# Kernel tuning notes

Hardware: AMD Instinct MI355X
Metric: run time of the kernel (lower is better)

The kernel has to match this reference:

```python
import jax, jax.numpy as jnp
import numpy as np

N_GENES = 20000
UNITS = 10000
DEG = 32
BATCH = 128

def setup_inputs() -> dict:
    key = jax.random.key(0)
    k1, k2, k3, k4 = jax.random.split(key, 4)
    feature = jax.random.normal(k1, (BATCH, N_GENES), dtype=jnp.float32)
    ppi = jax.random.randint(k2, (UNITS, DEG), 0, N_GENES, dtype=jnp.int64)
    kernel = jax.random.normal(k3, (UNITS,), dtype=jnp.float32)
    bias = jax.random.normal(k4, (UNITS,), dtype=jnp.float32)
    return {"feature": feature, "ppi": ppi, "kernel": kernel, "bias": bias}

def reference(feature, ppi, kernel, bias):
    # gather along gene axis: [B, UNITS, DEG]
    h = jnp.abs(feature[:, ppi])
    # sum over neighbors -> [B, UNITS]
    h = jnp.sum(h, axis=-1)
    h = h * kernel + bias
    return jnp.tanh(h)
```

## Files before the change

### kernel.cpp

```cpp
#include <hip/hip_runtime.h>
#include <hip/hip_fp16.h>
#include <math.h>

#define N_GENES 20000
#define UNITS   10000
#define DEG     32
#define BATCH   128

__global__ __launch_bounds__(256) void transpose_abs_f16_kernel(
    const float* __restrict__ in, __half* __restrict__ out)
{
    __shared__ float tile[32][33];
    const int g0 = blockIdx.x * 32;
    const int b0 = blockIdx.y * 32;
    const int tx = threadIdx.x;
    const int ty = threadIdx.y;
#pragma unroll
    for (int i = 0; i < 32; i += 8)
        tile[ty + i][tx] = fabsf(in[(size_t)(b0 + ty + i) * N_GENES + (g0 + tx)]);
    __syncthreads();
#pragma unroll
    for (int i = 0; i < 32; i += 8)
        out[(size_t)(g0 + ty + i) * BATCH + (b0 + tx)] = __float2half(tile[tx][ty + i]);
}

__global__ __launch_bounds__(256) void gather_unit_kernel(
    const __half2* __restrict__ featT,
    const int*   __restrict__ ppi,
    const float* __restrict__ kernelw,
    const float* __restrict__ bias,
    float*       __restrict__ out)
{
    __shared__ int idx[8 * DEG];
    const int tid = threadIdx.x;
    const int u0  = blockIdx.x * 8;

    idx[tid] = ppi[(size_t)u0 * DEG + tid];
    __syncthreads();

    const int lane = tid & 63;
    const int w    = tid >> 6;
    const int ub   = w * 2;

    float2 acc0 = {0.f, 0.f}, acc1 = {0.f, 0.f};

#pragma unroll 8
    for (int d = 0; d < DEG; ++d) {
        const int g0 = idx[ub * DEG + d];
        const int g1 = idx[(ub + 1) * DEG + d];
        const float2 f0 = __half22float2(featT[(size_t)g0 * 64 + lane]);
        const float2 f1 = __half22float2(featT[(size_t)g1 * 64 + lane]);
        acc0.x += f0.x; acc0.y += f0.y;
        acc1.x += f1.x; acc1.y += f1.y;
    }

    const int u  = u0 + ub;
    const float k0 = kernelw[u],     k1 = kernelw[u + 1];
    const float c0 = bias[u],        c1 = bias[u + 1];

    const float h00 = acc0.x * k0 + c0;
    const float h01 = acc1.x * k1 + c1;
    const float h10 = acc0.y * k0 + c0;
    const float h11 = acc1.y * k1 + c1;
    const float r00 = 1.f - 2.f / (__expf(2.f * h00) + 1.f);
    const float r01 = 1.f - 2.f / (__expf(2.f * h01) + 1.f);
    const float r10 = 1.f - 2.f / (__expf(2.f * h10) + 1.f);
    const float r11 = 1.f - 2.f / (__expf(2.f * h11) + 1.f);

    const int b = lane * 2;
    *(float2*)(out + (size_t)b       * UNITS + u) = make_float2(r00, r01);
    *(float2*)(out + (size_t)(b + 1) * UNITS + u) = make_float2(r10, r11);
}

extern "C" void kernel_launch(void* const* d_in, const int* in_sizes, int n_in,
                              void* d_out, int out_size, void* d_ws, size_t ws_size,
                              hipStream_t stream) {
    const float* feature = (const float*)d_in[0];
    const int*   ppi     = (const int*)d_in[1];
    const float* kernelw = (const float*)d_in[2];
    const float* bias    = (const float*)d_in[3];
    float* out   = (float*)d_out;
    __half* featT = (__half*)d_ws;

    dim3 g1(N_GENES / 32, BATCH / 32);
    dim3 b1(32, 8);
    transpose_abs_f16_kernel<<<g1, b1, 0, stream>>>(feature, featT);

    gather_unit_kernel<<<UNITS / 8, 256, 0, stream>>>(
        (const __half2*)featT, ppi, kernelw, bias, out);
}
```

Measured before the change: 78.83 us.

## Split transposed features into batch halves and gather with 8-byte loads per lane

```diff
diff --git a/kernel.cpp b/kernel.cpp
--- a/kernel.cpp
+++ b/kernel.cpp
@@ -6,6 +6,7 @@
 #define UNITS   10000
 #define DEG     32
 #define BATCH   128
+
 
 __global__ __launch_bounds__(256) void transpose_abs_f16_kernel(
     const float* __restrict__ in, __half* __restrict__ out)
@@ -19,12 +20,17 @@
     for (int i = 0; i < 32; i += 8)
         tile[ty + i][tx] = fabsf(in[(size_t)(b0 + ty + i) * N_GENES + (g0 + tx)]);
     __syncthreads();
+    const int b  = b0 + tx;
+    const int p  = b >> 6;
+    const int bh = b & 63;
 #pragma unroll
-    for (int i = 0; i < 32; i += 8)
-        out[(size_t)(g0 + ty + i) * BATCH + (b0 + tx)] = __float2half(tile[tx][ty + i]);
+    for (int i = 0; i < 32; i += 8) {
+        const int g = g0 + ty + i;
+        out[((size_t)p * N_GENES + g) * 64 + bh] = __float2half(tile[tx][ty + i]);
+    }
 }
 
-__global__ __launch_bounds__(256) void gather_unit_kernel(
+__global__ __launch_bounds__(256) void gather_unit_v3(
     const __half2* __restrict__ featT,
     const int*   __restrict__ ppi,
     const float* __restrict__ kernelw,
@@ -40,36 +46,44 @@
 
     const int lane = tid & 63;
     const int w    = tid >> 6;
-    const int ub   = w * 2;
+    const int dpar = lane >> 5;
+    const int ul   = w * 2 + ((lane >> 4) & 1);
+    const int bq   = lane & 15;
+    const int u    = u0 + ul;
+    const float kk = kernelw[u];
+    const float cc = bias[u];
+    const int* myidx = idx + ul * DEG;
 
-    float2 acc0 = {0.f, 0.f}, acc1 = {0.f, 0.f};
+#pragma unroll
+    for (int p = 0; p < 2; ++p) {
+        const uint2* fp = reinterpret_cast<const uint2*>(featT) + (size_t)p * N_GENES * 16;
+        float acc0 = 0.f, acc1 = 0.f, acc2 = 0.f, acc3 = 0.f;
+#pragma unroll
+        for (int t = 0; t < 16; ++t) {
+            const int d = 2 * t + dpar;
+            const int g = myidx[d];
+            const uint2 raw = fp[(size_t)g * 16 + bq];
+            const float2 f0 = __half22float2(*reinterpret_cast<const __half2*>(&raw.x));
+            const float2 f1 = __half22float2(*reinterpret_cast<const __half2*>(&raw.y));
+            acc0 += f0.x; acc1 += f0.y; acc2 += f1.x; acc3 += f1.y;
+        }
+        acc0 += __shfl_xor(acc0, 32, 64);
+        acc1 += __shfl_xor(acc1, 32, 64);
+        acc2 += __shfl_xor(acc2, 32, 64);
+        acc3 += __shfl_xor(acc3, 32, 64);
 
-#pragma unroll 8
-    for (int d = 0; d < DEG; ++d) {
-        const int g0 = idx[ub * DEG + d];
-        const int g1 = idx[(ub + 1) * DEG + d];
-        const float2 f0 = __half22float2(featT[(size_t)g0 * 64 + lane]);
-        const float2 f1 = __half22float2(featT[(size_t)g1 * 64 + lane]);
-        acc0.x += f0.x; acc0.y += f0.y;
-        acc1.x += f1.x; acc1.y += f1.y;
+        if (dpar == 0) {
+            const int bbase = p * 64 + bq * 4;
+            const float h0 = acc0 * kk + cc;
+            const float h1 = acc1 * kk + cc;
+            const float h2 = acc2 * kk + cc;
+            const float h3 = acc3 * kk + cc;
+            out[(size_t)(bbase + 0) * UNITS + u] = 1.f - 2.f / (__expf(2.f * h0) + 1.f);
+            out[(size_t)(bbase + 1) * UNITS + u] = 1.f - 2.f / (__expf(2.f * h1) + 1.f);
+            out[(size_t)(bbase + 2) * UNITS + u] = 1.f - 2.f / (__expf(2.f * h2) + 1.f);
+            out[(size_t)(bbase + 3) * UNITS + u] = 1.f - 2.f / (__expf(2.f * h3) + 1.f);
+        }
     }
-
-    const int u  = u0 + ub;
-    const float k0 = kernelw[u],     k1 = kernelw[u + 1];
-    const float c0 = bias[u],        c1 = bias[u + 1];
-
-    const float h00 = acc0.x * k0 + c0;
-    const float h01 = acc1.x * k1 + c1;
-    const float h10 = acc0.y * k0 + c0;
-    const float h11 = acc1.y * k1 + c1;
-    const float r00 = 1.f - 2.f / (__expf(2.f * h00) + 1.f);
-    const float r01 = 1.f - 2.f / (__expf(2.f * h01) + 1.f);
-    const float r10 = 1.f - 2.f / (__expf(2.f * h10) + 1.f);
-    const float r11 = 1.f - 2.f / (__expf(2.f * h11) + 1.f);
-
-    const int b = lane * 2;
-    *(float2*)(out + (size_t)b       * UNITS + u) = make_float2(r00, r01);
-    *(float2*)(out + (size_t)(b + 1) * UNITS + u) = make_float2(r10, r11);
 }
 
 extern "C" void kernel_launch(void* const* d_in, const int* in_sizes, int n_in,
@@ -86,6 +100,6 @@
     dim3 b1(32, 8);
     transpose_abs_f16_kernel<<<g1, b1, 0, stream>>>(feature, featT);
 
-    gather_unit_kernel<<<UNITS / 8, 256, 0, stream>>>(
+    gather_unit_v3<<<UNITS / 8, 256, 0, stream>>>(
         (const __half2*)featT, ppi, kernelw, bias, out);
 }
```

Result: no change. 78.57 us (-0.3%).

## Fuse abs/fp16 conversion into gather by staging batch-row pairs in LDS

Applied to the files above, without the earlier changes.

```diff
diff --git a/kernel.cpp b/kernel.cpp
--- a/kernel.cpp
+++ b/kernel.cpp
@@ -7,69 +7,59 @@
 #define DEG     32
 #define BATCH   128
 
-__global__ __launch_bounds__(256) void transpose_abs_f16_kernel(
-    const float* __restrict__ in, __half* __restrict__ out)
-{
-    __shared__ float tile[32][33];
-    const int g0 = blockIdx.x * 32;
-    const int b0 = blockIdx.y * 32;
-    const int tx = threadIdx.x;
-    const int ty = threadIdx.y;
-#pragma unroll
-    for (int i = 0; i < 32; i += 8)
-        tile[ty + i][tx] = fabsf(in[(size_t)(b0 + ty + i) * N_GENES + (g0 + tx)]);
-    __syncthreads();
-#pragma unroll
-    for (int i = 0; i < 32; i += 8)
-        out[(size_t)(g0 + ty + i) * BATCH + (b0 + tx)] = __float2half(tile[tx][ty + i]);
-}
+#define SPLIT   4
+#define UPC     (UNITS / SPLIT)
 
-__global__ __launch_bounds__(256) void gather_unit_kernel(
-    const __half2* __restrict__ featT,
+__global__ __launch_bounds__(256) void fused_ppi_v5(
+    const float* __restrict__ feature,
     const int*   __restrict__ ppi,
     const float* __restrict__ kernelw,
     const float* __restrict__ bias,
     float*       __restrict__ out)
 {
-    __shared__ int idx[8 * DEG];
-    const int tid = threadIdx.x;
-    const int u0  = blockIdx.x * 8;
+    extern __shared__ __half2 row2[];
+    const int t  = threadIdx.x;
+    const int p  = blockIdx.x / SPLIT;
+    const int c  = blockIdx.x % SPLIT;
+    const int b0 = p * 2, b1 = b0 + 1;
 
-    idx[tid] = ppi[(size_t)u0 * DEG + tid];
+    const float4* r0 = reinterpret_cast<const float4*>(feature + (size_t)b0 * N_GENES);
+    const float4* r1 = reinterpret_cast<const float4*>(feature + (size_t)b1 * N_GENES);
+    for (int g4 = t; g4 < N_GENES / 4; g4 += 256) {
+        const float4 a = r0[g4];
+        const float4 b = r1[g4];
+        __half2 h[4];
+        h[0] = __floats2half2_rn(fabsf(a.x), fabsf(b.x));
+        h[1] = __floats2half2_rn(fabsf(a.y), fabsf(b.y));
+        h[2] = __floats2half2_rn(fabsf(a.z), fabsf(b.z));
+        h[3] = __floats2half2_rn(fabsf(a.w), fabsf(b.w));
+        *reinterpret_cast<uint4*>(&row2[g4 * 4]) = *reinterpret_cast<const uint4*>(h);
+    }
     __syncthreads();
 
-    const int lane = tid & 63;
-    const int w    = tid >> 6;
-    const int ub   = w * 2;
+    for (int u = c * UPC + t; u < (c + 1) * UPC; u += 256) {
+        const uint4* pp = reinterpret_cast<const uint4*>(ppi + (size_t)u * DEG);
+        uint4 iv[8];
+#pragma unroll
+        for (int j = 0; j < 8; ++j) iv[j] = pp[j];
 
-    float2 acc0 = {0.f, 0.f}, acc1 = {0.f, 0.f};
+        float sx = 0.f, sy = 0.f;
+#pragma unroll
+        for (int j = 0; j < 8; ++j) {
+            const float2 f0 = __half22float2(row2[iv[j].x]);
+            const float2 f1 = __half22float2(row2[iv[j].y]);
+            const float2 f2 = __half22float2(row2[iv[j].z]);
+            const float2 f3 = __half22float2(row2[iv[j].w]);
+            sx += f0.x + f1.x + f2.x + f3.x;
+            sy += f0.y + f1.y + f2.y + f3.y;
+        }
 
-#pragma unroll 8
-    for (int d = 0; d < DEG; ++d) {
-        const int g0 = idx[ub * DEG + d];
-        const int g1 = idx[(ub + 1) * DEG + d];
-        const float2 f0 = __half22float2(featT[(size_t)g0 * 64 + lane]);
-        const float2 f1 = __half22float2(featT[(size_t)g1 * 64 + lane]);
-        acc0.x += f0.x; acc0.y += f0.y;
-        acc1.x += f1.x; acc1.y += f1.y;
+        const float kk = kernelw[u], cc = bias[u];
+        const float h0 = sx * kk + cc;
+        const float h1 = sy * kk + cc;
+        out[(size_t)b0 * UNITS + u] = 1.f - 2.f / (__expf(2.f * h0) + 1.f);
+        out[(size_t)b1 * UNITS + u] = 1.f - 2.f / (__expf(2.f * h1) + 1.f);
     }
-
-    const int u  = u0 + ub;
-    const float k0 = kernelw[u],     k1 = kernelw[u + 1];
-    const float c0 = bias[u],        c1 = bias[u + 1];
-
-    const float h00 = acc0.x * k0 + c0;
-    const float h01 = acc1.x * k1 + c1;
-    const float h10 = acc0.y * k0 + c0;
-    const float h11 = acc1.y * k1 + c1;
-    const float r00 = 1.f - 2.f / (__expf(2.f * h00) + 1.f);
-    const float r01 = 1.f - 2.f / (__expf(2.f * h01) + 1.f);
-    const float r10 = 1.f - 2.f / (__expf(2.f * h10) + 1.f);
-    const float r11 = 1.f - 2.f / (__expf(2.f * h11) + 1.f);
-
-    const int b = lane * 2;
-    *(float2*)(out + (size_t)b       * UNITS + u) = make_float2(r00, r01);
-    *(float2*)(out + (size_t)(b + 1) * UNITS + u) = make_float2(r10, r11);
 }
 
 extern "C" void kernel_launch(void* const* d_in, const int* in_sizes, int n_in,
@@ -80,12 +70,8 @@
     const float* kernelw = (const float*)d_in[2];
     const float* bias    = (const float*)d_in[3];
     float* out   = (float*)d_out;
-    __half* featT = (__half*)d_ws;
 
-    dim3 g1(N_GENES / 32, BATCH / 32);
-    dim3 b1(32, 8);
-    transpose_abs_f16_kernel<<<g1, b1, 0, stream>>>(feature, featT);
-
-    gather_unit_kernel<<<UNITS / 8, 256, 0, stream>>>(
-        (const __half2*)featT, ppi, kernelw, bias, out);
+    const dim3 grid((BATCH / 2) * SPLIT);
+    fused_ppi_v5<<<grid, 256, N_GENES * sizeof(__half2), stream>>>(
+        feature, ppi, kernelw, bias, out);
 }
```

Result: slower. 80.99 us (+2.7%).
